# Optimization experiments

Measured on AMD Instinct MI355X. Metric: run time of the kernel, lower is better.

The kernel has to match this reference:

```python
import jax, jax.numpy as jnp
import numpy as np

U, I, C, D, A, L, E = 40000, 40000, 5, 128, 64, 2, 1280000
N = U + I  # total graph nodes (users + items)
NEG_SLOPE = 0.01  # torch LeakyReLU default


def setup_inputs() -> dict:
    key = jax.random.key(0)
    ks = jax.random.split(key, 12)
    s = 0.05  # xavier-like scale
    return {
        "user_embed": jax.random.normal(ks[0], (U, C, D), jnp.float32) * s,
        "item_embed": jax.random.normal(ks[1], (I, C, D), jnp.float32) * s,
        "crit_embed": jax.random.normal(ks[2], (C, D), jnp.float32) * s,
        "gcn_weight": jax.random.normal(ks[3], (D, D), jnp.float32) * s,
        "gcn_layers": jax.random.normal(ks[4], (L, D, D), jnp.float32) * s,
        "crit_layers": jax.random.normal(ks[5], (L, D, D), jnp.float32) * s,
        "attn_p1": jax.random.normal(ks[6], (C, D, A), jnp.float32) * s,
        "attn_p2": jax.random.normal(ks[7], (C, A), jnp.float32) * s,
        "vals": jax.random.uniform(ks[8], (C, E), jnp.float32) / 16.0,
        "rows": jax.random.randint(ks[9], (C, E), 0, N, dtype=jnp.int32),
        "cols": jax.random.randint(ks[10], (C, E), 0, N, dtype=jnp.int32),
    }


def _forward(user_embed, item_embed, crit_embed, gcn_weight, gcn_layers,
             crit_layers, attn_p1, attn_p2, vals, rows, cols):
    ego = jnp.concatenate([user_embed, item_embed], axis=0)  # [N,C,D]
    bank = ego
    crit_hist = [crit_embed]  # list of [C,D], one per layer depth
    for l in range(L):
        crit_vec = crit_hist[l]  # [C,D]
        # per-criterion sparse adjacency matmul: A_c @ ego[:,c,:]
        feats = []
        for c in range(C):  # fixed small criterion count
            msg = vals[c][:, None] * jnp.take(ego[:, c, :], cols[c], axis=0)  # [E,D]
            feats.append(jax.ops.segment_sum(msg, rows[c], num_segments=N))
        gf = jnp.stack(feats, axis=1)                             # [N,C,D]
        gf = jnp.einsum('ncd,de->nce', gf, gcn_weight)            # dense GCN transform
        combined = gf * crit_vec[None, :, :]                      # criterion gating
        stacked = jax.nn.leaky_relu(
            jnp.einsum('ncd,de->nce', combined, gcn_layers[l]), NEG_SLOPE)  # [N,C,D]
        # tanh-attention aggregation, batched over the C output heads (k)
        h = jnp.tanh(jnp.einsum('ncd,kda->knca', stacked, attn_p1))  # [C,N,C,A]
        raw = jnp.einsum('knca,ka->knc', h, attn_p2)                 # [C,N,C]
        w = jax.nn.softmax(raw, axis=-1)                             # softmax over criteria
        ego = jnp.einsum('knc,ncd->nkd', w, stacked)                 # [N,C,D]
        bank = bank + ego
        crit_hist.append(crit_hist[l] @ crit_layers[l])  # [C,D]
    bank = bank / (L + 1)
    user_out = bank[:U]                                          # [U,C,D]
    item_out = jnp.concatenate(
        [bank[U:], jnp.zeros((1, C, D), bank.dtype)], axis=0)    # [I+1,C,D] dummy token
    crit_means = jnp.mean(jnp.stack(crit_hist, axis=0), axis=0)  # [C,D]
    return user_out, item_out, crit_means


def reference(user_embed, item_embed, crit_embed, gcn_weight, gcn_layers,
              crit_layers, attn_p1, attn_p2, vals, rows, cols):
    return _forward(user_embed, item_embed, crit_embed, gcn_weight, gcn_layers,
                    crit_layers, attn_p1, attn_p2, vals, rows, cols)
```

## Files before the change

### kernel.cpp

```cpp
#include <hip/hip_runtime.h>
#include <cstdint>
#include <cmath>

#define U_ 40000
#define I_ 40000
#define C_ 5
#define D_ 128
#define A_ 64
#define L_ 2
#define E_ 1280000
#define N_ (U_ + I_)
#define BINS_ (N_ * C_)
#define NEDGE_ (C_ * E_)
#define EPB_ 4096
#define NBRX_ ((NEDGE_ + EPB_ - 1) / EPB_)
#define ND1_ 1024
#define ND2_ 512

typedef __attribute__((ext_vector_type(8))) short short8;
typedef __attribute__((ext_vector_type(4))) short short4v;
typedef __attribute__((ext_vector_type(4))) float f32x4;

static __device__ __forceinline__ short f2bf(float f) {
    union { float f; uint32_t u; } x; x.f = f;
    uint32_t u = x.u;
    uint32_t r = (u + 0x7fffu + ((u >> 16) & 1u)) >> 16;
    return (short)r;
}

__global__ __launch_bounds__(256) void init_kernel(
    const float* __restrict__ user, const float* __restrict__ item,
    short* __restrict__ egob)
{
    size_t i = (size_t)blockIdx.x * 256 + threadIdx.x;
    const size_t total8 = (size_t)N_ * C_ * D_ / 8;
    const size_t user4  = (size_t)U_ * C_ * D_ / 4;
    if (i < total8) {
        size_t f4 = 2 * i;
        const float4* src = (f4 < user4) ? (const float4*)user
                                         : (const float4*)item - user4;
        float4 x0 = src[f4], x1 = src[f4 + 1];
        short8 p;
        p[0] = f2bf(x0.x); p[1] = f2bf(x0.y); p[2] = f2bf(x0.z); p[3] = f2bf(x0.w);
        p[4] = f2bf(x1.x); p[5] = f2bf(x1.y); p[6] = f2bf(x1.z); p[7] = f2bf(x1.w);
        ((short8*)egob)[i] = p;
    }
}

__global__ __launch_bounds__(128) void crit_kernel(
    const float* __restrict__ crit0, const float* __restrict__ clayers,
    float* __restrict__ crit1, float* __restrict__ crit2,
    float* __restrict__ crit_means, float* __restrict__ padrow)
{
    __shared__ float c0[C_ * D_], c1[C_ * D_], c2[C_ * D_];
    int t = threadIdx.x;
    for (int i = t; i < C_ * D_; i += 128) { c0[i] = crit0[i]; padrow[i] = 0.f; }
    __syncthreads();
    for (int c = 0; c < C_; ++c) {
        float acc = 0.f;
        for (int d = 0; d < D_; ++d) acc = fmaf(c0[c * D_ + d], clayers[d * D_ + t], acc);
        c1[c * D_ + t] = acc;
    }
    __syncthreads();
    for (int c = 0; c < C_; ++c) {
        float acc = 0.f;
        for (int d = 0; d < D_; ++d) acc = fmaf(c1[c * D_ + d], clayers[D_ * D_ + d * D_ + t], acc);
        c2[c * D_ + t] = acc;
    }
    __syncthreads();
    for (int i = t; i < C_ * D_; i += 128) {
        crit1[i] = c1[i];
        crit2[i] = c2[i];
        crit_means[i] = (c0[i] + c1[i] + c2[i]) * (1.0f / 3.0f);
    }
}

__global__ __launch_bounds__(256) void prepack_kernel(
    const float* __restrict__ W, const float* __restrict__ gl,
    short* __restrict__ Wf, short* __restrict__ Gf)
{
    int b = blockIdx.x;
    int m = b >> 3, t = b & 7;
    int q = threadIdx.x >> 6, l = threadIdx.x & 63;
    int g = l >> 4, c15 = l & 15;
    const float* src = (m == 0) ? W : gl + (size_t)(m - 1) * D_ * D_;
    short*       dst = (m == 0) ? Wf : Gf + (size_t)(m - 1) * D_ * D_;
    short8 v;
    #pragma unroll
    for (int j = 0; j < 8; ++j) {
        int k = q * 32 + g * 8 + j;
        int n = t * 16 + c15;
        v[j] = f2bf(src[k * D_ + n]);
    }
    *(short8*)(dst + (((t * 4 + q) * 64 + l) << 3)) = v;
}

__global__ __launch_bounds__(64) void prepack_p1_kernel(
    const float* __restrict__ p1, short* __restrict__ P1f)
{
    int t = blockIdx.x >> 2, q = blockIdx.x & 3;
    int lane = threadIdx.x;
    int g = lane >> 4, c15 = lane & 15;
    int k = t >> 2, a = (t & 3) * 16 + c15;
    short8 v;
    #pragma unroll
    for (int j = 0; j < 8; ++j) {
        int d = q * 32 + g * 8 + j;
        v[j] = f2bf(p1[((size_t)k * D_ + d) * A_ + a]);
    }
    *(short8*)(P1f + (((t * 4 + q) * 64 + lane) << 3)) = v;
}


__global__ __launch_bounds__(256) void p1_count_kernel(
    const int* __restrict__ rows, int* __restrict__ ghistT)
{
    __shared__ int h[ND1_];
    int b = blockIdx.x, tid = threadIdx.x;
    for (int i = tid; i < ND1_; i += 256) h[i] = 0;
    __syncthreads();
    int base = b * EPB_;
    for (int ch = 0; ch < EPB_ / 256; ++ch) {
        int eid = base + ch * 256 + tid;
        if (eid < NEDGE_) {
            int key = (eid / E_) * N_ + rows[eid];
            atomicAdd(&h[key & (ND1_ - 1)], 1);
        }
    }
    __syncthreads();
    for (int i = tid; i < ND1_; i += 256) ghistT[b * ND1_ + i] = h[i];
}

__global__ __launch_bounds__(256) void transpose_kernel(
    const int* __restrict__ src, int* __restrict__ dst, int R, int Cc)
{
    int i = blockIdx.x * 256 + threadIdx.x;
    if (i < R * Cc) { int r = i / Cc, c = i % Cc; dst[c * R + r] = src[i]; }
}

__global__ __launch_bounds__(256) void scanA_g(
    const int* __restrict__ src, int* __restrict__ dst,
    int* __restrict__ bsum, int n)
{
    __shared__ int ls[256];
    int b = blockIdx.x, t = threadIdx.x;
    int base = b * 1024 + t * 4;
    int v[4];
    #pragma unroll
    for (int i = 0; i < 4; ++i) v[i] = (base + i < n) ? src[base + i] : 0;
    int s = v[0] + v[1] + v[2] + v[3];
    ls[t] = s;
    __syncthreads();
    for (int off = 1; off < 256; off <<= 1) {
        int x = (t >= off) ? ls[t - off] : 0;
        __syncthreads();
        ls[t] += x;
        __syncthreads();
    }
    int excl = ls[t] - s;
    if (t == 255) bsum[b] = ls[255];
    #pragma unroll
    for (int i = 0; i < 4; ++i) {
        if (base + i < n) dst[base + i] = excl;
        excl += v[i];
    }
}

__global__ __launch_bounds__(256) void scanB_g(int* __restrict__ bsum, int nb)
{
    __shared__ int ls[256];
    int t = threadIdx.x;
    int v[8]; int s = 0;
    #pragma unroll
    for (int i = 0; i < 8; ++i) {
        int idx = t * 8 + i;
        v[i] = (idx < nb) ? bsum[idx] : 0;
        s += v[i];
    }
    ls[t] = s;
    __syncthreads();
    for (int off = 1; off < 256; off <<= 1) {
        int x = (t >= off) ? ls[t - off] : 0;
        __syncthreads();
        ls[t] += x;
        __syncthreads();
    }
    int excl = ls[t] - s;
    #pragma unroll
    for (int i = 0; i < 8; ++i) {
        int idx = t * 8 + i;
        if (idx < nb) bsum[idx] = excl;
        excl += v[i];
    }
}

__global__ __launch_bounds__(256) void scanC_g(
    int* __restrict__ dst, const int* __restrict__ bsum, int n)
{
    int b = blockIdx.x, t = threadIdx.x;
    int off = bsum[b];
    int base = b * 1024 + t * 4;
    #pragma unroll
    for (int i = 0; i < 4; ++i)
        if (base + i < n) dst[base + i] += off;
}

__global__ __launch_bounds__(256) void p1_place_kernel(
    const int* __restrict__ rows, const float* __restrict__ vals,
    const int* __restrict__ cols, const int* __restrict__ gbaseT,
    int* __restrict__ keyA, uint2* __restrict__ vcA)
{
    __shared__ int cur[ND1_];
    __shared__ int bst[ND1_];
    __shared__ int gb[ND1_];
    __shared__ int ts[256];
    __shared__ int sK[EPB_];
    __shared__ uint2 sV[EPB_];
    int b = blockIdx.x, tid = threadIdx.x;
    for (int i = tid; i < ND1_; i += 256) { cur[i] = 0; gb[i] = gbaseT[b * ND1_ + i]; }
    __syncthreads();
    int base = b * EPB_;
    for (int ch = 0; ch < EPB_ / 256; ++ch) {
        int eid = base + ch * 256 + tid;
        if (eid < NEDGE_) {
            int key = (eid / E_) * N_ + rows[eid];
            atomicAdd(&cur[key & (ND1_ - 1)], 1);
        }
    }
    __syncthreads();
    {
        int v[4]; int s = 0;
        #pragma unroll
        for (int i = 0; i < 4; ++i) { v[i] = cur[tid * 4 + i]; s += v[i]; }
        ts[tid] = s;
        __syncthreads();
        for (int off = 1; off < 256; off <<= 1) {
            int x = (tid >= off) ? ts[tid - off] : 0;
            __syncthreads();
            ts[tid] += x;
            __syncthreads();
        }
        int excl = ts[tid] - s;
        #pragma unroll
        for (int i = 0; i < 4; ++i) { bst[tid * 4 + i] = excl; excl += v[i]; }
        __syncthreads();
        #pragma unroll
        for (int i = 0; i < 4; ++i) cur[tid * 4 + i] = bst[tid * 4 + i];
    }
    __syncthreads();
    for (int ch = 0; ch < EPB_ / 256; ++ch) {
        int eid = base + ch * 256 + tid;
        if (eid < NEDGE_) {
            int key = (eid / E_) * N_ + rows[eid];
            int d = key & (ND1_ - 1);
            int p = atomicAdd(&cur[d], 1);
            sK[p] = key;
            union { float f; uint32_t u; } t; t.f = vals[eid];
            uint2 m; m.x = t.u; m.y = (uint32_t)cols[eid];
            sV[p] = m;
        }
    }
    __syncthreads();
    int M = NEDGE_ - base; if (M > EPB_) M = EPB_;
    for (int i = tid; i < M; i += 256) {
        int key = sK[i]; int d = key & (ND1_ - 1);
        int pos = gb[d] + (i - bst[d]);
        keyA[pos] = key; vcA[pos] = sV[i];
    }
}

__global__ __launch_bounds__(256) void p2_count_kernel(
    const int* __restrict__ keyA, int* __restrict__ ghistT)
{
    __shared__ int h[ND2_];
    int b = blockIdx.x, tid = threadIdx.x;
    for (int i = tid; i < ND2_; i += 256) h[i] = 0;
    __syncthreads();
    int base = b * EPB_;
    for (int ch = 0; ch < EPB_ / 256; ++ch) {
        int eid = base + ch * 256 + tid;
        if (eid < NEDGE_) atomicAdd(&h[keyA[eid] >> 10], 1);
    }
    __syncthreads();
    for (int i = tid; i < ND2_; i += 256) ghistT[b * ND2_ + i] = h[i];
}

__global__ __launch_bounds__(256) void p2_place_kernel(
    const int* __restrict__ keyA, const uint2* __restrict__ vcA,
    const int* __restrict__ gbaseT,
    int* __restrict__ keyB, uint2* __restrict__ vcB)
{
    __shared__ int cur[ND2_];
    __shared__ int bst[ND2_];
    __shared__ int gb[ND2_];
    __shared__ int wh[4 * ND2_];
    __shared__ int ts[256];
    __shared__ int sK[EPB_];
    __shared__ uint2 sV[EPB_];
    int b = blockIdx.x, tid = threadIdx.x;
    int lane = tid & 63, wv = tid >> 6;
    for (int i = tid; i < ND2_; i += 256) { cur[i] = 0; gb[i] = gbaseT[b * ND2_ + i]; }
    __syncthreads();
    int base = b * EPB_;
    for (int ch = 0; ch < EPB_ / 256; ++ch) {
        int eid = base + ch * 256 + tid;
        if (eid < NEDGE_) atomicAdd(&cur[keyA[eid] >> 10], 1);
    }
    __syncthreads();
    {
        int v0 = cur[tid * 2], v1 = cur[tid * 2 + 1];
        int s = v0 + v1;
        ts[tid] = s;
        __syncthreads();
        for (int off = 1; off < 256; off <<= 1) {
            int x = (tid >= off) ? ts[tid - off] : 0;
            __syncthreads();
            ts[tid] += x;
            __syncthreads();
        }
        int excl = ts[tid] - s;
        bst[tid * 2] = excl; bst[tid * 2 + 1] = excl + v0;
        __syncthreads();
        cur[tid * 2] = bst[tid * 2]; cur[tid * 2 + 1] = bst[tid * 2 + 1];
    }
    __syncthreads();
    for (int ch = 0; ch < EPB_ / 256; ++ch) {
        for (int i = tid; i < 4 * ND2_; i += 256) wh[i] = 0;
        __syncthreads();
        int eid = base + ch * 256 + tid;
        bool valid = eid < NEDGE_;
        int key = 0, d = 0; uint2 v = make_uint2(0u, 0u);
        if (valid) { key = keyA[eid]; v = vcA[eid]; d = key >> 10; }
        unsigned long long m = __ballot(valid ? 1 : 0);
        #pragma unroll
        for (int bit = 0; bit < 9; ++bit) {
            unsigned long long bb = __ballot((valid && ((d >> bit) & 1)) ? 1 : 0);
            m &= ((d >> bit) & 1) ? bb : ~bb;
        }
        unsigned long long ltm = ((unsigned long long)1 << lane) - 1;
        int rw = __popcll(m & ltm);
        int cnt = __popcll(m);
        if (valid && rw == 0) wh[wv * ND2_ + d] = cnt;
        __syncthreads();
        if (valid) {
            int off = 0;
            for (int w2 = 0; w2 < wv; ++w2) off += wh[w2 * ND2_ + d];
            int p = cur[d] + off + rw;
            sK[p] = key; sV[p] = v;
        }
        __syncthreads();
        for (int i = tid; i < ND2_; i += 256)
            cur[i] += wh[i] + wh[ND2_ + i] + wh[2 * ND2_ + i] + wh[3 * ND2_ + i];
        __syncthreads();
    }
    int M = NEDGE_ - base; if (M > EPB_) M = EPB_;
    for (int i = tid; i < M; i += 256) {
        int key = sK[i]; int d = key >> 10;
        int pos = gb[d] + (i - bst[d]);
        keyB[pos] = key; vcB[pos] = sV[i];
    }
}

__global__ __launch_bounds__(256) void boundary_kernel(
    const int* __restrict__ keyB, int* __restrict__ bin_start)
{
    int i = blockIdx.x * 256 + threadIdx.x;
    if (i >= NEDGE_) return;
    int k = keyB[i];
    if (i == 0) {
        for (int b = 0; b <= k; ++b) bin_start[b] = 0;
    } else {
        int kp = keyB[i - 1];
        for (int b = kp + 1; b <= k; ++b) bin_start[b] = i;
    }
    if (i == NEDGE_ - 1) {
        for (int b = k + 1; b <= BINS_; ++b) bin_start[b] = NEDGE_;
    }
}

__global__ __launch_bounds__(256) void gather_kernel(
    const uint4* __restrict__ eg128, const uint2* __restrict__ vc,
    const int* __restrict__ bin_start, uint4* __restrict__ gfb128)
{
    int w = (int)(((size_t)blockIdx.x * 256 + threadIdx.x) >> 6);
    int lane = threadIdx.x & 63;
    w = __builtin_amdgcn_readfirstlane(w);
    int bs = bin_start[w], be = bin_start[w + 1];
    int c = w / N_;
    int row = w - c * N_;
    int q4 = lane >> 4, l15 = lane & 15;
    float a0 = 0.f, a1 = 0.f, a2 = 0.f, a3 = 0.f;
    float a4 = 0.f, a5 = 0.f, a6 = 0.f, a7 = 0.f;

    for (int base = bs; base < be; base += 64) {
        int cnt = be - base; if (cnt > 64) cnt = 64;
        float v = 0.f; int s = 0;
        if (lane < cnt) {
            uint2 m = vc[base + lane];
            union { uint32_t u; float f; } t; t.u = m.x;
            v = t.f; s = (int)m.y;
        }
        int j = 0;
        for (; j + 16 <= cnt; j += 16) {
            float v0 = __shfl(v, j + q4),      v1 = __shfl(v, j + 4 + q4);
            float v2 = __shfl(v, j + 8 + q4),  v3 = __shfl(v, j + 12 + q4);
            int   s0 = __shfl(s, j + q4),      s1 = __shfl(s, j + 4 + q4);
            int   s2 = __shfl(s, j + 8 + q4),  s3 = __shfl(s, j + 12 + q4);
            uint4 m0 = eg128[((size_t)s0 * C_ + c) * (D_ / 8) + l15];
            uint4 m1 = eg128[((size_t)s1 * C_ + c) * (D_ / 8) + l15];
            uint4 m2 = eg128[((size_t)s2 * C_ + c) * (D_ / 8) + l15];
            uint4 m3 = eg128[((size_t)s3 * C_ + c) * (D_ / 8) + l15];
            union { uint32_t u; float f; } t;
            #define ACC8(mm, vv) \
                t.u = mm.x << 16;         a0 = fmaf(vv, t.f, a0); \
                t.u = mm.x & 0xffff0000u; a1 = fmaf(vv, t.f, a1); \
                t.u = mm.y << 16;         a2 = fmaf(vv, t.f, a2); \
                t.u = mm.y & 0xffff0000u; a3 = fmaf(vv, t.f, a3); \
                t.u = mm.z << 16;         a4 = fmaf(vv, t.f, a4); \
                t.u = mm.z & 0xffff0000u; a5 = fmaf(vv, t.f, a5); \
                t.u = mm.w << 16;         a6 = fmaf(vv, t.f, a6); \
                t.u = mm.w & 0xffff0000u; a7 = fmaf(vv, t.f, a7);
            ACC8(m0, v0) ACC8(m1, v1) ACC8(m2, v2) ACC8(m3, v3)
        }
        for (; j < cnt; j += 4) {
            float v0 = __shfl(v, j + q4);
            int   s0 = __shfl(s, j + q4);
            uint4 m0 = eg128[((size_t)s0 * C_ + c) * (D_ / 8) + l15];
            union { uint32_t u; float f; } t;
            ACC8(m0, v0)
            #undef ACC8
        }
    }
    a0 += __shfl_xor(a0, 16); a1 += __shfl_xor(a1, 16);
    a2 += __shfl_xor(a2, 16); a3 += __shfl_xor(a3, 16);
    a4 += __shfl_xor(a4, 16); a5 += __shfl_xor(a5, 16);
    a6 += __shfl_xor(a6, 16); a7 += __shfl_xor(a7, 16);
    a0 += __shfl_xor(a0, 32); a1 += __shfl_xor(a1, 32);
    a2 += __shfl_xor(a2, 32); a3 += __shfl_xor(a3, 32);
    a4 += __shfl_xor(a4, 32); a5 += __shfl_xor(a5, 32);
    a6 += __shfl_xor(a6, 32); a7 += __shfl_xor(a7, 32);
    if (lane < 16) {
        uint4 o;
        o.x = (uint32_t)(uint16_t)f2bf(a0) | ((uint32_t)(uint16_t)f2bf(a1) << 16);
        o.y = (uint32_t)(uint16_t)f2bf(a2) | ((uint32_t)(uint16_t)f2bf(a3) << 16);
        o.z = (uint32_t)(uint16_t)f2bf(a4) | ((uint32_t)(uint16_t)f2bf(a5) << 16);
        o.w = (uint32_t)(uint16_t)f2bf(a6) | ((uint32_t)(uint16_t)f2bf(a7) << 16);
        gfb128[((size_t)row * C_ + c) * (D_ / 8) + l15] = o;
    }
}

__global__ __launch_bounds__(1024, 4) void rowgemm_mfma_kernel(
    const short* __restrict__ gfb, short* __restrict__ stkb,
    const short* __restrict__ Wf, const short* __restrict__ Gf,
    const float* __restrict__ critv)
{
    __shared__ short Wl[16384];
    __shared__ short Gl[16384];
    __shared__ short Zr[16][2048];

    for (int i = threadIdx.x; i < 2048; i += 1024) {
        ((short8*)Wl)[i] = ((const short8*)Wf)[i];
        ((short8*)Gl)[i] = ((const short8*)Gf)[i];
    }
    __syncthreads();

    int lane = threadIdx.x & 63, w = threadIdx.x >> 6;
    int g = lane >> 4, c15 = lane & 15;
    char* zw = (char*)&Zr[w][0];
    const int nrb = (N_ * C_ + 255) / 256;

    for (int rb = blockIdx.x; rb < nrb; rb += gridDim.x) {
        size_t r0 = (size_t)rb * 256 + (size_t)w * 16;
        if (r0 >= N_ * C_) continue;

        short8 af[4];
        #pragma unroll
        for (int q = 0; q < 4; ++q)
            af[q] = *(const short8*)(gfb + (r0 + c15) * D_ + q * 32 + g * 8);

        f32x4 acc[8];
        #pragma unroll
        for (int t = 0; t < 8; ++t) acc[t] = (f32x4){0.f, 0.f, 0.f, 0.f};
        {
            const short8* Wp = (const short8*)Wl;
            #pragma unroll
            for (int t = 0; t < 8; ++t)
                #pragma unroll
                for (int q = 0; q < 4; ++q)
                    acc[t] = __builtin_amdgcn_mfma_f32_16x16x32_bf16(
                        af[q], Wp[(t * 4 + q) * 64 + lane], acc[t], 0, 0, 0);
        }

        int rbase = (int)r0 + g * 4;
        #pragma unroll
        for (int t = 0; t < 8; ++t)
            #pragma unroll
            for (int r = 0; r < 4; ++r) {
                float cv = critv[((rbase + r) % C_) * D_ + t * 16 + c15];
                float z = acc[t][r] * cv;
                int zrow = g * 4 + r;
                int cb = 32 * t + 2 * c15;
                int off = zrow * 256 + (cb ^ ((zrow & 7) << 4));
                *(short*)(zw + off) = f2bf(z);
            }

        short8 az[4];
        #pragma unroll
        for (int q = 0; q < 4; ++q) {
            int cb0 = 64 * q + 16 * g;
            int off = c15 * 256 + (cb0 ^ ((c15 & 7) << 4));
            az[q] = *(const short8*)(zw + off);
        }

        f32x4 acc2[8];
        #pragma unroll
        for (int t = 0; t < 8; ++t) acc2[t] = (f32x4){0.f, 0.f, 0.f, 0.f};
        {
            const short8* Gp = (const short8*)Gl;
            #pragma unroll
            for (int t = 0; t < 8; ++t)
                #pragma unroll
                for (int q = 0; q < 4; ++q)
                    acc2[t] = __builtin_amdgcn_mfma_f32_16x16x32_bf16(
                        az[q], Gp[(t * 4 + q) * 64 + lane], acc2[t], 0, 0, 0);
        }

        #pragma unroll
        for (int t = 0; t < 8; ++t)
            #pragma unroll
            for (int r = 0; r < 4; ++r) {
                float s = acc2[t][r];
                s = s > 0.f ? s : 0.01f * s;
                int zrow = g * 4 + r;
                int cb = 32 * t + 2 * c15;
                int off = zrow * 256 + (cb ^ ((zrow & 7) << 4));
                *(short*)(zw + off) = f2bf(s);
            }
        #pragma unroll
        for (int q = 0; q < 4; ++q) {
            int cb0 = 64 * q + 16 * g;
            int off = c15 * 256 + (cb0 ^ ((c15 & 7) << 4));
            short8 sv = *(const short8*)(zw + off);
            *(short8*)(stkb + (r0 + c15) * D_ + q * 32 + g * 8) = sv;
        }
    }
}

__global__ __launch_bounds__(256, 3) void attn_mfma_kernel(
    const short* __restrict__ stkb, const short* __restrict__ P1f,
    const float* __restrict__ p2, const float* __restrict__ user,
    const float* __restrict__ item, short* __restrict__ egob,
    float* __restrict__ bank, int last)
{
    __shared__ float rawl[80 * C_];
    __shared__ float wl[80 * C_];

    int tid = threadIdx.x;
    int lane = tid & 63, w = tid >> 6;
    int g = lane >> 4, c15 = lane & 15;
    int klo = (5 * w) >> 2;

    short8 Bf[5][4];
    float p2v[5];
    #pragma unroll
    for (int i = 0; i < 5; ++i) {
        int t = 5 * w + i;
        #pragma unroll
        for (int q = 0; q < 4; ++q)
            Bf[i][q] = ((const short8*)P1f)[(t * 4 + q) * 64 + lane];
        p2v[i] = p2[(t >> 2) * A_ + (t & 3) * 16 + c15];
    }

    float4*       bank4 = (float4*)bank;
    const float4* user4 = (const float4*)user;
    const float4* item4 = (const float4*)item;

    for (int grp = blockIdx.x; grp < N_ / 16; grp += gridDim.x) {
        size_t n0 = (size_t)grp * 16;
        for (int i = tid; i < 80 * C_; i += 256) rawl[i] = 0.f;
        __syncthreads();

        for (int rt = 0; rt < 5; ++rt) {
            short8 af[4];
            #pragma unroll
            for (int q = 0; q < 4; ++q)
                af[q] = *(const short8*)(stkb + (n0 * 5 + rt * 16 + c15) * D_ + q * 32 + g * 8);

            f32x4 acc[5];
            #pragma unroll
            for (int i = 0; i < 5; ++i) acc[i] = (f32x4){0.f, 0.f, 0.f, 0.f};
            #pragma unroll
            for (int i = 0; i < 5; ++i)
                #pragma unroll
                for (int q = 0; q < 4; ++q)
                    acc[i] = __builtin_amdgcn_mfma_f32_16x16x32_bf16(
                        af[q], Bf[i][q], acc[i], 0, 0, 0);

            float2 ps[4];
            #pragma unroll
            for (int r = 0; r < 4; ++r) ps[r] = make_float2(0.f, 0.f);
            #pragma unroll
            for (int i = 0; i < 5; ++i) {
                int t = 5 * w + i;
                bool lo = (t >> 2) == klo;
                #pragma unroll
                for (int r = 0; r < 4; ++r) {
                    float x = acc[i][r];
                    float e = __expf(2.f * x);
                    float th = 1.f - 2.f * __builtin_amdgcn_rcpf(e + 1.f);
                    float con = th * p2v[i];
                    if (lo) ps[r].x += con; else ps[r].y += con;
                }
            }
            #pragma unroll
            for (int r = 0; r < 4; ++r) {
                #pragma unroll
                for (int m = 1; m < 16; m <<= 1) {
                    ps[r].x += __shfl_xor(ps[r].x, m);
                    ps[r].y += __shfl_xor(ps[r].y, m);
                }
                if (c15 == 0) {
                    int row = rt * 16 + g * 4 + r;
                    atomicAdd(&rawl[row * C_ + klo], ps[r].x);
                    atomicAdd(&rawl[row * C_ + klo + 1], ps[r].y);
                }
            }
        }
        __syncthreads();

        if (tid < 80) {
            int nl = tid / C_, k = tid % C_;
            float rv[C_];
            #pragma unroll
            for (int c = 0; c < C_; ++c) rv[c] = rawl[(nl * C_ + c) * C_ + k];
            float m = rv[0];
            #pragma unroll
            for (int c = 1; c < C_; ++c) m = fmaxf(m, rv[c]);
            float s = 0.f;
            #pragma unroll
            for (int c = 0; c < C_; ++c) { rv[c] = __expf(rv[c] - m); s += rv[c]; }
            float inv = __builtin_amdgcn_rcpf(s);
            #pragma unroll
            for (int c = 0; c < C_; ++c) wl[tid * C_ + c] = rv[c] * inv;
        }
        __syncthreads();

        #pragma unroll
        for (int ii = 0; ii < 10; ++ii) {
            int idx = tid + 256 * ii;
            int f4 = idx & 31;
            int nl = (idx >> 5) & 15, k = idx >> 9;
            float4 a = make_float4(0.f, 0.f, 0.f, 0.f);
            #pragma unroll
            for (int c = 0; c < C_; ++c) {
                float wv = wl[(nl * C_ + k) * C_ + c];
                uint2 sv = ((const uint2*)(stkb + ((n0 + nl) * C_ + c) * D_))[f4];
                union { uint32_t u; float f; } t;
                t.u = sv.x << 16;         a.x = fmaf(wv, t.f, a.x);
                t.u = sv.x & 0xffff0000u; a.y = fmaf(wv, t.f, a.y);
                t.u = sv.y << 16;         a.z = fmaf(wv, t.f, a.z);
                t.u = sv.y & 0xffff0000u; a.w = fmaf(wv, t.f, a.w);
            }
            size_t n = n0 + nl;
            size_t go = (n * 5 + k) * 32 + f4;
            if (!last) {
                short4v pk;
                pk[0] = f2bf(a.x); pk[1] = f2bf(a.y); pk[2] = f2bf(a.z); pk[3] = f2bf(a.w);
                *(short4v*)(egob + go * 4) = pk;
            } else {
                uint2 e0 = *(const uint2*)(egob + go * 4);
                union { uint32_t u; float f; } t;
                float4 b = (n < U_) ? user4[((size_t)n * C_ + k) * 32 + f4]
                                    : item4[((size_t)(n - U_) * C_ + k) * 32 + f4];
                t.u = e0.x << 16;         b.x += t.f + a.x;
                t.u = e0.x & 0xffff0000u; b.y += t.f + a.y;
                t.u = e0.y << 16;         b.z += t.f + a.z;
                t.u = e0.y & 0xffff0000u; b.w += t.f + a.w;
                b.x *= (1.f / 3.f); b.y *= (1.f / 3.f);
                b.z *= (1.f / 3.f); b.w *= (1.f / 3.f);
                bank4[go] = b;
            }
        }
    }
}

extern "C" void kernel_launch(void* const* d_in, const int* in_sizes, int n_in,
                              void* d_out, int out_size, void* d_ws, size_t ws_size,
                              hipStream_t stream) {
    const float* user  = (const float*)d_in[0];
    const float* item  = (const float*)d_in[1];
    const float* crit0 = (const float*)d_in[2];
    const float* W     = (const float*)d_in[3];
    const float* gl    = (const float*)d_in[4];
    const float* cl    = (const float*)d_in[5];
    const float* p1    = (const float*)d_in[6];
    const float* p2    = (const float*)d_in[7];
    const float* vals  = (const float*)d_in[8];
    const int*   rows  = (const int*)d_in[9];
    const int*   cols  = (const int*)d_in[10];

    float* out  = (float*)d_out;
    float* bank = out;
    float* padrow = out + (size_t)N_ * C_ * D_;
    float* crit_means = out + (size_t)(N_ + 1) * C_ * D_;

    const size_t NCD = (size_t)N_ * C_ * D_;
    short* egob  = (short*)d_ws;
    short* gfb   = egob + NCD;
    short* stkb  = gfb + NCD;
    float* crit1 = (float*)(stkb + NCD);
    float* crit2 = crit1 + C_ * D_;
    short* Wf    = (short*)(crit2 + C_ * D_);
    short* Gf    = Wf + (size_t)D_ * D_;
    short* P1f   = Gf + 2 * (size_t)D_ * D_;
    int* bin_start = (int*)(P1f + (size_t)D_ * C_ * A_);
    int* keyB      = bin_start + BINS_ + 2;
    uint2* vcB     = (uint2*)(keyB + NEDGE_);
    int* ghist     = (int*)(vcB + NEDGE_);
    int* ghistT    = ghist + (size_t)ND1_ * NBRX_;
    int* bsum      = ghistT + (size_t)ND1_ * NBRX_;
    uint2* vcA = (uint2*)stkb;
    int*  keyA = (int*)((char*)stkb + (size_t)NEDGE_ * 8);

    init_kernel<<<(int)((NCD / 8 + 255) / 256), 256, 0, stream>>>(user, item, egob);
    crit_kernel<<<1, 128, 0, stream>>>(crit0, cl, crit1, crit2, crit_means, padrow);
    prepack_kernel<<<24, 256, 0, stream>>>(W, gl, Wf, Gf);
    prepack_p1_kernel<<<80, 64, 0, stream>>>(p1, P1f);

    const int n1 = ND1_ * NBRX_, n2 = ND2_ * NBRX_;
    p1_count_kernel<<<NBRX_, 256, 0, stream>>>(rows, ghistT);
    transpose_kernel<<<(n1 + 255) / 256, 256, 0, stream>>>(ghistT, ghist, NBRX_, ND1_);
    scanA_g<<<(n1 + 1023) / 1024, 256, 0, stream>>>(ghist, ghist, bsum, n1);
    scanB_g<<<1, 256, 0, stream>>>(bsum, (n1 + 1023) / 1024);
    scanC_g<<<(n1 + 1023) / 1024, 256, 0, stream>>>(ghist, bsum, n1);
    transpose_kernel<<<(n1 + 255) / 256, 256, 0, stream>>>(ghist, ghistT, ND1_, NBRX_);
    p1_place_kernel<<<NBRX_, 256, 0, stream>>>(rows, vals, cols, ghistT, keyA, vcA);

    p2_count_kernel<<<NBRX_, 256, 0, stream>>>(keyA, ghistT);
    transpose_kernel<<<(n2 + 255) / 256, 256, 0, stream>>>(ghistT, ghist, NBRX_, ND2_);
    scanA_g<<<(n2 + 1023) / 1024, 256, 0, stream>>>(ghist, ghist, bsum, n2);
    scanB_g<<<1, 256, 0, stream>>>(bsum, (n2 + 1023) / 1024);
    scanC_g<<<(n2 + 1023) / 1024, 256, 0, stream>>>(ghist, bsum, n2);
    transpose_kernel<<<(n2 + 255) / 256, 256, 0, stream>>>(ghist, ghistT, ND2_, NBRX_);
    p2_place_kernel<<<NBRX_, 256, 0, stream>>>(keyA, vcA, ghistT, keyB, vcB);

    boundary_kernel<<<(NEDGE_ + 255) / 256, 256, 0, stream>>>(keyB, bin_start);

    for (int l = 0; l < L_; ++l) {
        gather_kernel<<<BINS_ / 4, 256, 0, stream>>>(
            (const uint4*)egob, vcB, bin_start, (uint4*)gfb);
        rowgemm_mfma_kernel<<<256, 1024, 0, stream>>>(
            gfb, stkb, Wf, Gf + (size_t)l * D_ * D_, l == 0 ? crit0 : crit1);
        attn_mfma_kernel<<<768, 256, 0, stream>>>(
            stkb, P1f, p2, user, item, egob, bank, l == L_ - 1 ? 1 : 0);
    }
}
```

Measured before the change: 1.310 ms.

## Simplify gather edge loads, store MFMA output directly, widen attention vector accesses

The sparse gather kernel now has each lane load its own edge (value, column) pair directly instead of loading a 64-edge batch and broadcasting with shuffles, which removes the cross-lane shuffle traffic. The transform kernel swaps the MFMA operands so each lane writes its accumulator row straight to global memory, skipping the swizzled LDS staging round-trip. The attention output loop moves to 16-byte loads and stores with 8 elements per thread. The cost is redundant edge-metadata loads across lane groups and less coalesced, narrower global stores from the transform kernel.

```diff
diff --git a/kernel.cpp b/kernel.cpp
--- a/kernel.cpp
+++ b/kernel.cpp
@@ -392,45 +392,45 @@
     float a0 = 0.f, a1 = 0.f, a2 = 0.f, a3 = 0.f;
     float a4 = 0.f, a5 = 0.f, a6 = 0.f, a7 = 0.f;
 
-    for (int base = bs; base < be; base += 64) {
-        int cnt = be - base; if (cnt > 64) cnt = 64;
-        float v = 0.f; int s = 0;
-        if (lane < cnt) {
-            uint2 m = vc[base + lane];
-            union { uint32_t u; float f; } t; t.u = m.x;
-            v = t.f; s = (int)m.y;
-        }
-        int j = 0;
-        for (; j + 16 <= cnt; j += 16) {
-            float v0 = __shfl(v, j + q4),      v1 = __shfl(v, j + 4 + q4);
-            float v2 = __shfl(v, j + 8 + q4),  v3 = __shfl(v, j + 12 + q4);
-            int   s0 = __shfl(s, j + q4),      s1 = __shfl(s, j + 4 + q4);
-            int   s2 = __shfl(s, j + 8 + q4),  s3 = __shfl(s, j + 12 + q4);
-            uint4 m0 = eg128[((size_t)s0 * C_ + c) * (D_ / 8) + l15];
-            uint4 m1 = eg128[((size_t)s1 * C_ + c) * (D_ / 8) + l15];
-            uint4 m2 = eg128[((size_t)s2 * C_ + c) * (D_ / 8) + l15];
-            uint4 m3 = eg128[((size_t)s3 * C_ + c) * (D_ / 8) + l15];
-            union { uint32_t u; float f; } t;
-            #define ACC8(mm, vv) \
-                t.u = mm.x << 16;         a0 = fmaf(vv, t.f, a0); \
-                t.u = mm.x & 0xffff0000u; a1 = fmaf(vv, t.f, a1); \
-                t.u = mm.y << 16;         a2 = fmaf(vv, t.f, a2); \
-                t.u = mm.y & 0xffff0000u; a3 = fmaf(vv, t.f, a3); \
-                t.u = mm.z << 16;         a4 = fmaf(vv, t.f, a4); \
-                t.u = mm.z & 0xffff0000u; a5 = fmaf(vv, t.f, a5); \
-                t.u = mm.w << 16;         a6 = fmaf(vv, t.f, a6); \
-                t.u = mm.w & 0xffff0000u; a7 = fmaf(vv, t.f, a7);
-            ACC8(m0, v0) ACC8(m1, v1) ACC8(m2, v2) ACC8(m3, v3)
-        }
-        for (; j < cnt; j += 4) {
-            float v0 = __shfl(v, j + q4);
-            int   s0 = __shfl(s, j + q4);
-            uint4 m0 = eg128[((size_t)s0 * C_ + c) * (D_ / 8) + l15];
-            union { uint32_t u; float f; } t;
-            ACC8(m0, v0)
-            #undef ACC8
-        }
-    }
+    union { uint32_t u; float f; } t;
+    #define ACC8(mm, vv) \
+        t.u = mm.x << 16;         a0 = fmaf(vv, t.f, a0); \
+        t.u = mm.x & 0xffff0000u; a1 = fmaf(vv, t.f, a1); \
+        t.u = mm.y << 16;         a2 = fmaf(vv, t.f, a2); \
+        t.u = mm.y & 0xffff0000u; a3 = fmaf(vv, t.f, a3); \
+        t.u = mm.z << 16;         a4 = fmaf(vv, t.f, a4); \
+        t.u = mm.z & 0xffff0000u; a5 = fmaf(vv, t.f, a5); \
+        t.u = mm.w << 16;         a6 = fmaf(vv, t.f, a6); \
+        t.u = mm.w & 0xffff0000u; a7 = fmaf(vv, t.f, a7);
+
+    int j = bs;
+    for (; j + 16 <= be; j += 16) {
+        uint2 eA = vc[j + q4];
+        uint2 eB = vc[j + 4 + q4];
+        uint2 eC = vc[j + 8 + q4];
+        uint2 eD = vc[j + 12 + q4];
+        uint4 mA = eg128[((size_t)(int)eA.y * C_ + c) * (D_ / 8) + l15];
+        uint4 mB = eg128[((size_t)(int)eB.y * C_ + c) * (D_ / 8) + l15];
+        uint4 mC = eg128[((size_t)(int)eC.y * C_ + c) * (D_ / 8) + l15];
+        uint4 mD = eg128[((size_t)(int)eD.y * C_ + c) * (D_ / 8) + l15];
+        union { uint32_t u; float f; } fv;
+        fv.u = eA.x; float vA = fv.f;
+        fv.u = eB.x; float vB = fv.f;
+        fv.u = eC.x; float vC = fv.f;
+        fv.u = eD.x; float vD = fv.f;
+        ACC8(mA, vA) ACC8(mB, vB) ACC8(mC, vC) ACC8(mD, vD)
+    }
+    for (; j < be; j += 4) {
+        int idx = j + q4;
+        bool act = idx < be;
+        uint2 e0 = vc[act ? idx : be - 1];
+        union { uint32_t u; float f; } fv; fv.u = e0.x;
+        float v0 = act ? fv.f : 0.f;
+        uint4 m0 = eg128[((size_t)(int)e0.y * C_ + c) * (D_ / 8) + l15];
+        ACC8(m0, v0)
+    }
+    #undef ACC8
+
     a0 += __shfl_xor(a0, 16); a1 += __shfl_xor(a1, 16);
     a2 += __shfl_xor(a2, 16); a3 += __shfl_xor(a3, 16);
     a4 += __shfl_xor(a4, 16); a5 += __shfl_xor(a5, 16);
@@ -522,26 +522,21 @@
                 #pragma unroll
                 for (int q = 0; q < 4; ++q)
                     acc2[t] = __builtin_amdgcn_mfma_f32_16x16x32_bf16(
-                        az[q], Gp[(t * 4 + q) * 64 + lane], acc2[t], 0, 0, 0);
-        }
-
-        #pragma unroll
-        for (int t = 0; t < 8; ++t)
-            #pragma unroll
-            for (int r = 0; r < 4; ++r) {
-                float s = acc2[t][r];
-                s = s > 0.f ? s : 0.01f * s;
-                int zrow = g * 4 + r;
-                int cb = 32 * t + 2 * c15;
-                int off = zrow * 256 + (cb ^ ((zrow & 7) << 4));
-                *(short*)(zw + off) = f2bf(s);
-            }
-        #pragma unroll
-        for (int q = 0; q < 4; ++q) {
-            int cb0 = 64 * q + 16 * g;
-            int off = c15 * 256 + (cb0 ^ ((c15 & 7) << 4));
-            short8 sv = *(const short8*)(zw + off);
-            *(short8*)(stkb + (r0 + c15) * D_ + q * 32 + g * 8) = sv;
+                        Gp[(t * 4 + q) * 64 + lane], az[q], acc2[t], 0, 0, 0);
+        }
+
+        short* srow = stkb + (r0 + c15) * D_;
+        #pragma unroll
+        for (int t = 0; t < 8; ++t) {
+            float s0 = acc2[t][0], s1 = acc2[t][1], s2 = acc2[t][2], s3 = acc2[t][3];
+            s0 = s0 > 0.f ? s0 : 0.01f * s0;
+            s1 = s1 > 0.f ? s1 : 0.01f * s1;
+            s2 = s2 > 0.f ? s2 : 0.01f * s2;
+            s3 = s3 > 0.f ? s3 : 0.01f * s3;
+            uint2 o;
+            o.x = (uint32_t)(uint16_t)f2bf(s0) | ((uint32_t)(uint16_t)f2bf(s1) << 16);
+            o.y = (uint32_t)(uint16_t)f2bf(s2) | ((uint32_t)(uint16_t)f2bf(s3) << 16);
+            *(uint2*)(srow + t * 16 + g * 4) = o;
         }
     }
 }
@@ -646,39 +641,54 @@
         __syncthreads();
 
         #pragma unroll
-        for (int ii = 0; ii < 10; ++ii) {
+        for (int ii = 0; ii < 5; ++ii) {
             int idx = tid + 256 * ii;
-            int f4 = idx & 31;
-            int nl = (idx >> 5) & 15, k = idx >> 9;
-            float4 a = make_float4(0.f, 0.f, 0.f, 0.f);
+            int f8 = idx & 15;
+            int nl = (idx >> 4) & 15, k = idx >> 8;
+            float e[8] = {0.f, 0.f, 0.f, 0.f, 0.f, 0.f, 0.f, 0.f};
             #pragma unroll
             for (int c = 0; c < C_; ++c) {
                 float wv = wl[(nl * C_ + k) * C_ + c];
-                uint2 sv = ((const uint2*)(stkb + ((n0 + nl) * C_ + c) * D_))[f4];
+                uint4 sv = ((const uint4*)(stkb + ((n0 + nl) * C_ + c) * D_))[f8];
                 union { uint32_t u; float f; } t;
-                t.u = sv.x << 16;         a.x = fmaf(wv, t.f, a.x);
-                t.u = sv.x & 0xffff0000u; a.y = fmaf(wv, t.f, a.y);
-                t.u = sv.y << 16;         a.z = fmaf(wv, t.f, a.z);
-                t.u = sv.y & 0xffff0000u; a.w = fmaf(wv, t.f, a.w);
+                t.u = sv.x << 16;         e[0] = fmaf(wv, t.f, e[0]);
+                t.u = sv.x & 0xffff0000u; e[1] = fmaf(wv, t.f, e[1]);
+                t.u = sv.y << 16;         e[2] = fmaf(wv, t.f, e[2]);
+                t.u = sv.y & 0xffff0000u; e[3] = fmaf(wv, t.f, e[3]);
+                t.u = sv.z << 16;         e[4] = fmaf(wv, t.f, e[4]);
+                t.u = sv.z & 0xffff0000u; e[5] = fmaf(wv, t.f, e[5]);
+                t.u = sv.w << 16;         e[6] = fmaf(wv, t.f, e[6]);
+                t.u = sv.w & 0xffff0000u; e[7] = fmaf(wv, t.f, e[7]);
             }
             size_t n = n0 + nl;
-            size_t go = (n * 5 + k) * 32 + f4;
+            size_t go = ((n * 5 + k) * 16 + f8) * 8;
             if (!last) {
-                short4v pk;
-                pk[0] = f2bf(a.x); pk[1] = f2bf(a.y); pk[2] = f2bf(a.z); pk[3] = f2bf(a.w);
-                *(short4v*)(egob + go * 4) = pk;
+                short8 pk;
+                #pragma unroll
+                for (int x = 0; x < 8; ++x) pk[x] = f2bf(e[x]);
+                *(short8*)(egob + go) = pk;
             } else {
-                uint2 e0 = *(const uint2*)(egob + go * 4);
+                uint4 e0 = *(const uint4*)(egob + go);
+                size_t bo = (n * 5 + k) * 32 + f8 * 2;
+                float4 b0 = (n < U_) ? user4[((size_t)n * C_ + k) * 32 + f8 * 2]
+                                     : item4[((size_t)(n - U_) * C_ + k) * 32 + f8 * 2];
+                float4 b1 = (n < U_) ? user4[((size_t)n * C_ + k) * 32 + f8 * 2 + 1]
+                                     : item4[((size_t)(n - U_) * C_ + k) * 32 + f8 * 2 + 1];
                 union { uint32_t u; float f; } t;
-                float4 b = (n < U_) ? user4[((size_t)n * C_ + k) * 32 + f4]
-                                    : item4[((size_t)(n - U_) * C_ + k) * 32 + f4];
-                t.u = e0.x << 16;         b.x += t.f + a.x;
-                t.u = e0.x & 0xffff0000u; b.y += t.f + a.y;
-                t.u = e0.y << 16;         b.z += t.f + a.z;
-                t.u = e0.y & 0xffff0000u; b.w += t.f + a.w;
-                b.x *= (1.f / 3.f); b.y *= (1.f / 3.f);
-                b.z *= (1.f / 3.f); b.w *= (1.f / 3.f);
-                bank4[go] = b;
+                t.u = e0.x << 16;         b0.x += t.f + e[0];
+                t.u = e0.x & 0xffff0000u; b0.y += t.f + e[1];
+                t.u = e0.y << 16;         b0.z += t.f + e[2];
+                t.u = e0.y & 0xffff0000u; b0.w += t.f + e[3];
+                t.u = e0.z << 16;         b1.x += t.f + e[4];
+                t.u = e0.z & 0xffff0000u; b1.y += t.f + e[5];
+                t.u = e0.w << 16;         b1.z += t.f + e[6];
+                t.u = e0.w & 0xffff0000u; b1.w += t.f + e[7];
+                b0.x *= (1.f / 3.f); b0.y *= (1.f / 3.f);
+                b0.z *= (1.f / 3.f); b0.w *= (1.f / 3.f);
+                b1.x *= (1.f / 3.f); b1.y *= (1.f / 3.f);
+                b1.z *= (1.f / 3.f); b1.w *= (1.f / 3.f);
+                bank4[bo] = b0;
+                bank4[bo + 1] = b1;
             }
         }
     }
```

Result: no change. 1.335 ms (+1.9%).
